# Kernel tuning notes

Measured on AMD Instinct MI355X. Metric: run time of the kernel, lower is better.

Reference implementation:

```python
import jax, jax.numpy as jnp
import numpy as np

TAU = 0.07  # args.density_tau

N, D = 8192, 768   # feature bank
B = 4096           # classify queries
P = 2048           # density peaks
C = 256            # num_class
K_NEIGH = 20       # args.density_k


def setup_inputs() -> dict:
    key = jax.random.key(0)
    k1, k2, k3, k4 = jax.random.split(key, 4)
    return {
        "features": jax.random.normal(k1, (N, D), dtype=jnp.float32),
        "h_i": jax.random.normal(k2, (B, D), dtype=jnp.float32),
        "peak_features": jax.random.normal(k3, (P, D), dtype=jnp.float32),
        "labels": jax.random.randint(k4, (P,), 0, C),
        "K": K_NEIGH,
        "num_class": C,
    }


def _l2norm(x):
    return x / jnp.linalg.norm(x, axis=-1, keepdims=True)


def reference(features, h_i, peak_features, labels, K, num_class):
    # ---- calculate_density_batch ----
    # cosine similarity of every row vs every row: [N, N]
    f = _l2norm(features)
    sim = f @ f.T
    # sort descending + keep K+1 == top_k(K+1); row i's best match is itself
    knn_sims, knn_idx = jax.lax.top_k(sim, K + 1)
    densities = knn_sims[:, 1:].mean(axis=1)   # [N], self excluded
    knn_indices = knn_idx[:, 1:]               # [N, K]
    # density peak test (vectorized find_density_peaks): i is a peak iff
    # its density exceeds all of its K neighbors' densities
    peak_mask = jnp.all(densities[:, None] > densities[knn_indices], axis=1)

    # ---- classify / soft_nearest_neighbor ----
    hn = _l2norm(h_i)
    pn = _l2norm(peak_features)  # cached peak features are L2-normalized
    logits = (hn @ pn.T) / TAU                     # [B, P]
    one_hot = jax.nn.one_hot(labels, num_class, dtype=logits.dtype)  # [P, C]
    # exp(logits) @ one_hot / sum(exp(logits)) == softmax(logits) @ one_hot
    preds = jax.nn.softmax(logits, axis=-1) @ one_hot  # [B, C]

    return preds, densities, knn_indices, peak_mask
```

## Files before the change

### kernel.cpp

```cpp
#include <hip/hip_runtime.h>
#include <math.h>

#define N_FEAT 8192
#define DIM    768
#define B_H    4096
#define P_PK   2048
#define C_CLS  256
#define KNN    20

#define OUT_DENS_OFF  (B_H * C_CLS)
#define OUT_KNN_OFF   (OUT_DENS_OFF + N_FEAT)
#define OUT_MASK_OFF  (OUT_KNN_OFF + N_FEAT * KNN)

typedef __attribute__((ext_vector_type(8)))  short short8b;
typedef __attribute__((ext_vector_type(16))) float f32x16;

__global__ __launch_bounds__(256) void norm64_kernel(const float* __restrict__ X,
    float* __restrict__ nrm, float* __restrict__ rn, int rows) {
  int w    = (int)((blockIdx.x * blockDim.x + threadIdx.x) >> 6);
  int lane = threadIdx.x & 63;
  if (w >= rows) return;
  const float* x = X + (size_t)w * DIM;
  double s = 0.0;
#pragma unroll
  for (int k = 0; k < 12; ++k) {
    float v = x[lane + 64 * k];
    s += (double)v * (double)v;
  }
#pragma unroll
  for (int off = 32; off; off >>= 1) s += __shfl_xor(s, off);
  if (lane == 0) {
    float n32 = (float)sqrt(s);
    nrm[w] = n32;
    rn[w]  = 1.0f / n32;
  }
}

__device__ inline unsigned short f2bf(float x) {
  unsigned u = __float_as_uint(x);
  return (unsigned short)((u + 0x7fffu + ((u >> 16) & 1u)) >> 16);
}

__global__ __launch_bounds__(256) void tobf16_kernel(const float* __restrict__ F,
    const float* __restrict__ rn, unsigned short* __restrict__ fnb) {
  int gid = (blockIdx.x * 256 + threadIdx.x) * 8;
  int row = gid / DIM;
  float s = rn[row];
  float4 v0 = *(const float4*)(F + gid);
  float4 v1 = *(const float4*)(F + gid + 4);
  uint4 o;
  o.x = (unsigned)f2bf(v0.x * s) | ((unsigned)f2bf(v0.y * s) << 16);
  o.y = (unsigned)f2bf(v0.z * s) | ((unsigned)f2bf(v0.w * s) << 16);
  o.z = (unsigned)f2bf(v1.x * s) | ((unsigned)f2bf(v1.y * s) << 16);
  o.w = (unsigned)f2bf(v1.z * s) | ((unsigned)f2bf(v1.w * s) << 16);
  *(uint4*)(fnb + gid) = o;
}

__global__ __launch_bounds__(256) void tofn32_kernel(const float* __restrict__ F,
    const float* __restrict__ nrm, float* __restrict__ fn32) {
#pragma clang fp contract(off)
  int gid = (blockIdx.x * 256 + threadIdx.x) * 4;
  int row = gid / DIM;
  float ni = nrm[row];
  float4 v = *(const float4*)(F + gid);
  v.x = v.x / ni; v.y = v.y / ni; v.z = v.z / ni; v.w = v.w / ni;
  *(float4*)(fn32 + gid) = v;
}

__global__ __launch_bounds__(512, 2) void sim_topk_mfma(
    const unsigned short* __restrict__ fnb, int* __restrict__ cand) {
  __shared__ __align__(16) uint4 Bs[2][128 * 17];
  __shared__ __align__(16) float simb[64][130];

  const int t  = threadIdx.x;
  const int l  = t & 63;
  const int w  = t >> 6;
  const int wr = w >> 2;
  const int wc = w & 3;
  const int rg = blockIdx.x >> 1;
  const int hg = blockIdx.x & 1;
  const int ib = rg * 64;
  const int jb0 = hg * 4096;

  const int lc = l & 31;
  const int lh = l >> 5;
  const int bsw = 4 * (lc & 3);

  const int scol = t >> 2;
  const int sq   = t & 3;
  const int wsw  = sq ^ (scol & 3);

  short8b a[48];
  {
    const unsigned short* ap = fnb + (size_t)(ib + wr * 32 + lc) * DIM + lh * 8;
#pragma unroll
    for (int kc = 0; kc < 48; ++kc) a[kc] = *(const short8b*)(ap + kc * 16);
  }

  const int h = l >> 5;
  const int q = l & 31;
  float lv[4], cmv[4];
  int   li[4];
#pragma unroll
  for (int p = 0; p < 4; ++p) { lv[p] = -3e38f; li[p] = 0; cmv[p] = -3e38f; }

  uint4 v0, v1, v2, v3;
  {
    const unsigned short* gb = fnb + (size_t)(jb0 + scol) * DIM + sq * 32;
    v0 = *(const uint4*)(gb);
    v1 = *(const uint4*)(gb + 8);
    v2 = *(const uint4*)(gb + 16);
    v3 = *(const uint4*)(gb + 24);
  }
  int cur = 0;

#pragma unroll 1
  for (int ct = 0; ct < 32; ++ct) {
    f32x16 acc;
#pragma unroll
    for (int i = 0; i < 16; ++i) acc[i] = 0.f;

#pragma unroll
    for (int kq = 0; kq < 6; ++kq) {
      {
        uint4* bd = &Bs[cur][scol * 17 + 4 * wsw];
        bd[0] = v0; bd[1] = v1; bd[2] = v2; bd[3] = v3;
      }
      __syncthreads();
      if (!(ct == 31 && kq == 5)) {
        const int nct = (kq == 5) ? ct + 1 : ct;
        const int nkq = (kq == 5) ? 0 : kq + 1;
        const unsigned short* gb =
            fnb + (size_t)(jb0 + nct * 128 + scol) * DIM + nkq * 128 + sq * 32;
        v0 = *(const uint4*)(gb);
        v1 = *(const uint4*)(gb + 8);
        v2 = *(const uint4*)(gb + 16);
        v3 = *(const uint4*)(gb + 24);
      }
#pragma unroll
      for (int s = 0; s < 8; ++s) {
        const int slot = (2 * s + lh) ^ bsw;
        const short8b b = *(const short8b*)&Bs[cur][(wc * 32 + lc) * 17 + slot];
        acc = __builtin_amdgcn_mfma_f32_32x32x16_bf16(a[kq * 8 + s], b, acc, 0, 0, 0);
      }
      cur ^= 1;
    }

#pragma unroll
    for (int reg = 0; reg < 16; ++reg) {
      simb[wr * 32 + (reg & 3) + 8 * (reg >> 2) + 4 * lh][wc * 32 + lc] = acc[reg];
    }
    __syncthreads();

    const int jbct = jb0 + ct * 128;
#pragma unroll
    for (int p = 0; p < 4; ++p) {
      const int r  = w * 8 + 2 * p + h;
      const int ig = ib + r;
#pragma unroll
      for (int s = 0; s < 4; ++s) {
        float v  = simb[r][32 * s + q];
        int   jj = jbct + 32 * s + q;
        bool pred = (v > cmv[p]) && (jj != ig);
        unsigned long long bm = __ballot(pred);
        unsigned hm = (unsigned)(bm >> (h * 32));
        while (hm) {
          const int lb = __ffs(hm) - 1;
          hm &= hm - 1;
          const float bv = __shfl(v,  h * 32 + lb);
          const int   bj = __shfl(jj, h * 32 + lb);
          if (bv > cmv[p]) {
            unsigned em = (unsigned)(__ballot(lv[p] == cmv[p]) >> (h * 32));
            if (q == __ffs(em) - 1) { lv[p] = bv; li[p] = bj; }
            float ov = lv[p];
#pragma unroll
            for (int d = 1; d <= 16; d <<= 1) ov = fminf(ov, __shfl_xor(ov, d));
            cmv[p] = ov;
          }
        }
      }
    }
  }

#pragma unroll
  for (int p = 0; p < 4; ++p) {
    const int ig = ib + w * 8 + 2 * p + h;
    cand[(size_t)ig * 64 + hg * 32 + q] = li[p];
  }
}

__global__ __launch_bounds__(256) void refine64_fn32(const float* __restrict__ fn32,
    const int* __restrict__ cand, float* __restrict__ dens, float* __restrict__ knnf) {
#pragma clang fp contract(off)
  const int i = blockIdx.x;
  const int t = threadIdx.x;
  const int l = t & 63;
  const int w = t >> 6;
  __shared__ __align__(16) float fni[DIM];
  __shared__ float s32v[64];
  __shared__ int   vidx[64];
  __shared__ float ssorted[KNN];

  const float* fni_g = fn32 + (size_t)i * DIM;
  for (int d = t; d < DIM; d += 256) fni[d] = fni_g[d];
  if (t < 64) vidx[t] = cand[(size_t)i * 64 + t];
  __syncthreads();

  for (int c = w * 16; c < w * 16 + 16; ++c) {
    const int j = vidx[c];
    const float* fj = fn32 + (size_t)j * DIM;
    double s = 0.0;
#pragma unroll
    for (int k2 = 0; k2 < 12; ++k2) {
      s += (double)fni[l + 64 * k2] * (double)fj[l + 64 * k2];
    }
#pragma unroll
    for (int off = 32; off; off >>= 1) s += __shfl_xor(s, off);
    if (l == 0) s32v[c] = (float)s;
  }
  __syncthreads();

  if (t < 64) {
    const float v = s32v[t];
    const int   j = vidx[t];
    int rank = 0;
    for (int k = 0; k < 64; ++k) {
      float vk = s32v[k]; int jk = vidx[k];
      rank += (vk > v || (vk == v && jk > j)) ? 1 : 0;
    }
    if (rank < KNN) {
      knnf[(size_t)i * KNN + rank] = (float)j;
      ssorted[rank] = v;
    }
  }
  __syncthreads();

  if (t == 0) {
    float rr[8];
#pragma unroll
    for (int u = 0; u < 8; ++u) rr[u] = ssorted[u];
#pragma unroll
    for (int u = 0; u < 8; ++u) rr[u] = rr[u] + ssorted[8 + u];
    float res = ((rr[0] + rr[1]) + (rr[2] + rr[3])) + ((rr[4] + rr[5]) + (rr[6] + rr[7]));
    res = res + ssorted[16];
    res = res + ssorted[17];
    res = res + ssorted[18];
    res = res + ssorted[19];
    dens[i] = res / 20.0f;
  }
}

__global__ __launch_bounds__(256) void refine64_div(const float* __restrict__ F,
    const float* __restrict__ nrm, const int* __restrict__ cand,
    float* __restrict__ dens, float* __restrict__ knnf) {
#pragma clang fp contract(off)
  const int i = blockIdx.x;
  const int t = threadIdx.x;
  const int l = t & 63;
  const int w = t >> 6;
  __shared__ __align__(16) float fni[DIM];
  __shared__ float s32v[64];
  __shared__ int   vidx[64];
  __shared__ float ssorted[KNN];

  const float ni = nrm[i];
  for (int d = t; d < DIM; d += 256) fni[d] = F[(size_t)i * DIM + d] / ni;
  if (t < 64) vidx[t] = cand[(size_t)i * 64 + t];
  __syncthreads();

  for (int c = w * 16; c < w * 16 + 16; ++c) {
    const int j = vidx[c];
    const float* fj = F + (size_t)j * DIM;
    const float nj = nrm[j];
    double s = 0.0;
#pragma unroll
    for (int k2 = 0; k2 < 12; ++k2) {
      float fjn = fj[l + 64 * k2] / nj;
      s += (double)fni[l + 64 * k2] * (double)fjn;
    }
#pragma unroll
    for (int off = 32; off; off >>= 1) s += __shfl_xor(s, off);
    if (l == 0) s32v[c] = (float)s;
  }
  __syncthreads();

  if (t < 64) {
    const float v = s32v[t];
    const int   j = vidx[t];
    int rank = 0;
    for (int k = 0; k < 64; ++k) {
      float vk = s32v[k]; int jk = vidx[k];
      rank += (vk > v || (vk == v && jk > j)) ? 1 : 0;
    }
    if (rank < KNN) {
      knnf[(size_t)i * KNN + rank] = (float)j;
      ssorted[rank] = v;
    }
  }
  __syncthreads();

  if (t == 0) {
    float rr[8];
#pragma unroll
    for (int u = 0; u < 8; ++u) rr[u] = ssorted[u];
#pragma unroll
    for (int u = 0; u < 8; ++u) rr[u] = rr[u] + ssorted[8 + u];
    float res = ((rr[0] + rr[1]) + (rr[2] + rr[3])) + ((rr[4] + rr[5]) + (rr[6] + rr[7]));
    res = res + ssorted[16];
    res = res + ssorted[17];
    res = res + ssorted[18];
    res = res + ssorted[19];
    dens[i] = res / 20.0f;
  }
}

__global__ __launch_bounds__(256) void peak_kernel(const float* __restrict__ dens,
    const float* __restrict__ knnf, float* __restrict__ mask) {
  int i = blockIdx.x * 256 + threadIdx.x;
  if (i >= N_FEAT) return;
  float di = dens[i];
  int ok = 1;
#pragma unroll
  for (int k = 0; k < KNN; ++k) {
    int j = (int)knnf[(size_t)i * KNN + k];
    ok &= (di > dens[j]) ? 1 : 0;
  }
  mask[i] = ok ? 1.0f : 0.0f;
}

__global__ __launch_bounds__(256) void preds_kernel(const float* __restrict__ H,
    const float* __restrict__ Pk, const int* __restrict__ labels,
    const float* __restrict__ rnh, const float* __restrict__ rnp,
    float* __restrict__ outp) {
  __shared__ __align__(16) float Hs[32][12];
  __shared__ __align__(16) float Ps[32][130];
  __shared__ float accc[8][C_CLS];

  const int t  = threadIdx.x;
  const int hb = blockIdx.x * 8;
  const int tx = t & 63;
  const int ry = t >> 6;
  const int hr  = t >> 5;
  const int hkk = t & 31;
  const int pr  = t >> 1;
  const int pkk = (t & 1) * 16;
  const float hrn = rnh[hb + hr];

  for (int i = t; i < 8 * C_CLS; i += 256) ((float*)accc)[i] = 0.f;

  float m[2]    = {-3e38f, -3e38f};
  float ssum[2] = {0.f, 0.f};
  __syncthreads();

  for (int pt = 0; pt < 16; ++pt) {
    const int pb = pt * 128;
    const float prn = rnp[pb + pr];
    float acc[2][2] = {{0.f, 0.f}, {0.f, 0.f}};

    for (int kc = 0; kc < 24; ++kc) {
      const int kb = kc * 32;
      __syncthreads();
      Hs[hkk][hr] = H[(size_t)(hb + hr) * DIM + kb + hkk] * hrn;
      {
        const float* src = Pk + (size_t)(pb + pr) * DIM + kb + pkk;
        float4 v0 = *(const float4*)(src);
        float4 v1 = *(const float4*)(src + 4);
        float4 v2 = *(const float4*)(src + 8);
        float4 v3 = *(const float4*)(src + 12);
        Ps[pkk +  0][pr] = v0.x * prn;  Ps[pkk +  1][pr] = v0.y * prn;
        Ps[pkk +  2][pr] = v0.z * prn;  Ps[pkk +  3][pr] = v0.w * prn;
        Ps[pkk +  4][pr] = v1.x * prn;  Ps[pkk +  5][pr] = v1.y * prn;
        Ps[pkk +  6][pr] = v1.z * prn;  Ps[pkk +  7][pr] = v1.w * prn;
        Ps[pkk +  8][pr] = v2.x * prn;  Ps[pkk +  9][pr] = v2.y * prn;
        Ps[pkk + 10][pr] = v2.z * prn;  Ps[pkk + 11][pr] = v2.w * prn;
        Ps[pkk + 12][pr] = v3.x * prn;  Ps[pkk + 13][pr] = v3.y * prn;
        Ps[pkk + 14][pr] = v3.z * prn;  Ps[pkk + 15][pr] = v3.w * prn;
      }
      __syncthreads();
#pragma unroll
      for (int k = 0; k < 32; ++k) {
        float2 a = *(const float2*)&Hs[k][2 * ry];
        float2 b = *(const float2*)&Ps[k][2 * tx];
        acc[0][0] += a.x * b.x; acc[0][1] += a.x * b.y;
        acc[1][0] += a.y * b.x; acc[1][1] += a.y * b.y;
      }
    }
    const int lab0 = labels[pb + 2 * tx];
    const int lab1 = labels[pb + 2 * tx + 1];
#pragma unroll
    for (int rr = 0; rr < 2; ++rr) {
      float l0 = acc[rr][0] / 0.07f;
      float l1 = acc[rr][1] / 0.07f;
      float tm = fmaxf(l0, l1);
#pragma unroll
      for (int off = 32; off; off >>= 1) tm = fmaxf(tm, __shfl_xor(tm, off));
      float mn = fmaxf(m[rr], tm);
      float sc = expf(m[rr] - mn);
      const int row = 2 * ry + rr;
#pragma unroll
      for (int qq = 0; qq < 4; ++qq) accc[row][tx + 64 * qq] *= sc;
      float e0 = expf(l0 - mn);
      float e1 = expf(l1 - mn);
      float es = e0 + e1;
#pragma unroll
      for (int off = 32; off; off >>= 1) es += __shfl_xor(es, off);
      ssum[rr] = ssum[rr] * sc + es;
      m[rr] = mn;
      atomicAdd(&accc[row][lab0], e0);
      atomicAdd(&accc[row][lab1], e1);
    }
  }
#pragma unroll
  for (int rr = 0; rr < 2; ++rr) {
    const int row = 2 * ry + rr;
    float inv = 1.0f / ssum[rr];
#pragma unroll
    for (int qq = 0; qq < 4; ++qq) {
      outp[(size_t)(hb + row) * C_CLS + tx + 64 * qq] = accc[row][tx + 64 * qq] * inv;
    }
  }
}

extern "C" void kernel_launch(void* const* d_in, const int* in_sizes, int n_in,
                              void* d_out, int out_size, void* d_ws, size_t ws_size,
                              hipStream_t stream) {
  (void)in_sizes; (void)n_in; (void)out_size;
  const float* F      = (const float*)d_in[0];
  const float* H      = (const float*)d_in[1];
  const float* Pk     = (const float*)d_in[2];
  const int*   labels = (const int*)d_in[3];
  float* out = (float*)d_out;

  float* ws   = (float*)d_ws;
  float* nrmF = ws;
  float* rnF  = nrmF + N_FEAT;
  float* nrmH = rnF + N_FEAT;
  float* rnH  = nrmH + B_H;
  float* nrmP = rnH + B_H;
  float* rnP  = nrmP + P_PK;
  int*   cand = (int*)(rnP + P_PK);
  unsigned short* fnb = (unsigned short*)(cand + N_FEAT * 64);
  float* fn32 = (float*)(fnb + (size_t)N_FEAT * DIM);
  const size_t need = (size_t)(fn32 - ws) * 4 + (size_t)N_FEAT * DIM * 4;
  const bool use_fn32 = ws_size >= need;

  norm64_kernel<<<N_FEAT / 4, 256, 0, stream>>>(F, nrmF, rnF, N_FEAT);
  norm64_kernel<<<B_H / 4,  256, 0, stream>>>(H, nrmH, rnH, B_H);
  norm64_kernel<<<P_PK / 4, 256, 0, stream>>>(Pk, nrmP, rnP, P_PK);

  tobf16_kernel<<<N_FEAT * DIM / (8 * 256), 256, 0, stream>>>(F, rnF, fnb);
  if (use_fn32) {
    tofn32_kernel<<<N_FEAT * DIM / (4 * 256), 256, 0, stream>>>(F, nrmF, fn32);
  }

  sim_topk_mfma<<<256, 512, 0, stream>>>(fnb, cand);

  if (use_fn32) {
    refine64_fn32<<<N_FEAT, 256, 0, stream>>>(fn32, cand,
        out + OUT_DENS_OFF, out + OUT_KNN_OFF);
  } else {
    refine64_div<<<N_FEAT, 256, 0, stream>>>(F, nrmF, cand,
        out + OUT_DENS_OFF, out + OUT_KNN_OFF);
  }

  peak_kernel<<<N_FEAT / 256, 256, 0, stream>>>(out + OUT_DENS_OFF,
      out + OUT_KNN_OFF, out + OUT_MASK_OFF);

  preds_kernel<<<B_H / 8, 256, 0, stream>>>(H, Pk, labels, rnH, rnP, out);
}
```

Baseline: 1.374 ms.

## Compute classifier logits with bf16 MFMA using hi/lo split queries

Replaces the scalar FP32 preds kernel with an MFMA-based kernel. Normalized queries are split into bf16 hi and lo parts, and peaks are cast to bf16. Logits are accumulated with two MFMAs per k-chunk, followed by an online softmax and an LDS atomic scatter into class bins. This moves the B×P×D dot products onto matrix cores, at the cost of reduced precision on the peak side and extra workspace and conversion kernels. It falls back to the old kernel when the workspace is too small.

```diff
diff --git a/kernel.cpp b/kernel.cpp
--- a/kernel.cpp
+++ b/kernel.cpp
@@ -13,6 +13,7 @@
 #define OUT_MASK_OFF  (OUT_KNN_OFF + N_FEAT * KNN)
 
 typedef __attribute__((ext_vector_type(8)))  short short8b;
+typedef __attribute__((ext_vector_type(4)))  float f32x4;
 typedef __attribute__((ext_vector_type(16))) float f32x16;
 
 __global__ __launch_bounds__(256) void norm64_kernel(const float* __restrict__ X,
@@ -39,6 +40,9 @@
 __device__ inline unsigned short f2bf(float x) {
   unsigned u = __float_as_uint(x);
   return (unsigned short)((u + 0x7fffu + ((u >> 16) & 1u)) >> 16);
+}
+__device__ inline float bf2f(unsigned short h) {
+  return __uint_as_float(((unsigned)h) << 16);
 }
 
 __global__ __launch_bounds__(256) void tobf16_kernel(const float* __restrict__ F,
@@ -54,6 +58,31 @@
   o.z = (unsigned)f2bf(v1.x * s) | ((unsigned)f2bf(v1.y * s) << 16);
   o.w = (unsigned)f2bf(v1.z * s) | ((unsigned)f2bf(v1.w * s) << 16);
   *(uint4*)(fnb + gid) = o;
+}
+
+__global__ __launch_bounds__(256) void split_kernel(const float* __restrict__ X,
+    const float* __restrict__ rn, unsigned short* __restrict__ hi,
+    unsigned short* __restrict__ lo) {
+  int gid = (blockIdx.x * 256 + threadIdx.x) * 8;
+  int row = gid / DIM;
+  float s = rn[row];
+  float4 v0 = *(const float4*)(X + gid);
+  float4 v1 = *(const float4*)(X + gid + 4);
+  float x[8] = {v0.x * s, v0.y * s, v0.z * s, v0.w * s,
+                v1.x * s, v1.y * s, v1.z * s, v1.w * s};
+  unsigned short h[8], l[8];
+#pragma unroll
+  for (int i = 0; i < 8; ++i) {
+    h[i] = f2bf(x[i]);
+    l[i] = f2bf(x[i] - bf2f(h[i]));
+  }
+  uint4 oh, ol;
+  oh.x = h[0] | ((unsigned)h[1] << 16); oh.y = h[2] | ((unsigned)h[3] << 16);
+  oh.z = h[4] | ((unsigned)h[5] << 16); oh.w = h[6] | ((unsigned)h[7] << 16);
+  ol.x = l[0] | ((unsigned)l[1] << 16); ol.y = l[2] | ((unsigned)l[3] << 16);
+  ol.z = l[4] | ((unsigned)l[5] << 16); ol.w = l[6] | ((unsigned)l[7] << 16);
+  *(uint4*)(hi + gid) = oh;
+  *(uint4*)(lo + gid) = ol;
 }
 
 __global__ __launch_bounds__(256) void tofn32_kernel(const float* __restrict__ F,
@@ -326,6 +355,110 @@
     ok &= (di > dens[j]) ? 1 : 0;
   }
   mask[i] = ok ? 1.0f : 0.0f;
+}
+
+__global__ __launch_bounds__(512) void preds_mfma(
+    const unsigned short* __restrict__ hh, const unsigned short* __restrict__ hl,
+    const unsigned short* __restrict__ ph, const int* __restrict__ labels,
+    float* __restrict__ outp) {
+  __shared__ __align__(16) unsigned short Bsh[2][128 * 40];
+  __shared__ __align__(16) float logit[16][132];
+  __shared__ float accc[16][C_CLS];
+  __shared__ int   labs[P_PK];
+
+  const int t  = threadIdx.x;
+  const int l  = t & 63;
+  const int w  = t >> 6;
+  const int hb = blockIdx.x * 16;
+  const int lr = l & 15;
+  const int lk = l >> 4;
+
+  short8b Ah[24], Al[24];
+  {
+    const unsigned short* hp = hh + (size_t)(hb + lr) * DIM + lk * 8;
+    const unsigned short* lp = hl + (size_t)(hb + lr) * DIM + lk * 8;
+#pragma unroll
+    for (int kc = 0; kc < 24; ++kc) {
+      Ah[kc] = *(const short8b*)(hp + kc * 32);
+      Al[kc] = *(const short8b*)(lp + kc * 32);
+    }
+  }
+
+  for (int i = t; i < P_PK; i += 512) labs[i] = labels[i];
+  for (int i = t; i < 16 * C_CLS; i += 512) ((float*)accc)[i] = 0.f;
+
+  float m0 = -3e38f, m1 = -3e38f, s0 = 0.f, s1 = 0.f;
+
+  const int scol = t >> 2;
+  const int sseg = t & 3;
+
+  uint4 pv = *(const uint4*)(ph + (size_t)scol * DIM + sseg * 8);
+  int cur = 0;
+  __syncthreads();
+
+#pragma unroll 1
+  for (int ct = 0; ct < 16; ++ct) {
+    f32x4 acc = {0.f, 0.f, 0.f, 0.f};
+
+#pragma unroll 1
+    for (int kc = 0; kc < 24; ++kc) {
+      *(uint4*)&Bsh[cur][scol * 40 + sseg * 8] = pv;
+      __syncthreads();
+      if (!(ct == 15 && kc == 23)) {
+        const int nct = (kc == 23) ? ct + 1 : ct;
+        const int nkc = (kc == 23) ? 0 : kc + 1;
+        pv = *(const uint4*)(ph + (size_t)(nct * 128 + scol) * DIM + nkc * 32 + sseg * 8);
+      }
+      const short8b b = *(const short8b*)&Bsh[cur][(16 * w + lr) * 40 + lk * 8];
+      acc = __builtin_amdgcn_mfma_f32_16x16x32_bf16(Ah[kc], b, acc, 0, 0, 0);
+      acc = __builtin_amdgcn_mfma_f32_16x16x32_bf16(Al[kc], b, acc, 0, 0, 0);
+      cur ^= 1;
+    }
+
+#pragma unroll
+    for (int reg = 0; reg < 4; ++reg) {
+      logit[lk * 4 + reg][16 * w + lr] = acc[reg] / 0.07f;
+    }
+    __syncthreads();
+
+    const int pb = ct * 128;
+    const int lab0 = labs[pb + l];
+    const int lab1 = labs[pb + 64 + l];
+#pragma unroll
+    for (int rr = 0; rr < 2; ++rr) {
+      const int r = 2 * w + rr;
+      float v0 = logit[r][l];
+      float v1 = logit[r][64 + l];
+      float tm = fmaxf(v0, v1);
+#pragma unroll
+      for (int off = 32; off; off >>= 1) tm = fmaxf(tm, __shfl_xor(tm, off));
+      float mo = rr ? m1 : m0;
+      float mn = fmaxf(mo, tm);
+      float sc = expf(mo - mn);
+#pragma unroll
+      for (int qq = 0; qq < 4; ++qq) accc[r][l + 64 * qq] *= sc;
+      float e0 = expf(v0 - mn);
+      float e1 = expf(v1 - mn);
+      float es = e0 + e1;
+#pragma unroll
+      for (int off = 32; off; off >>= 1) es += __shfl_xor(es, off);
+      if (rr) { s1 = s1 * sc + es; m1 = mn; }
+      else    { s0 = s0 * sc + es; m0 = mn; }
+      atomicAdd(&accc[r][lab0], e0);
+      atomicAdd(&accc[r][lab1], e1);
+    }
+    __syncthreads();
+  }
+
+#pragma unroll
+  for (int rr = 0; rr < 2; ++rr) {
+    const int r = 2 * w + rr;
+    const float inv = 1.0f / (rr ? s1 : s0);
+#pragma unroll
+    for (int qq = 0; qq < 4; ++qq) {
+      outp[(size_t)(hb + r) * C_CLS + l + 64 * qq] = accc[r][l + 64 * qq] * inv;
+    }
+  }
 }
 
 __global__ __launch_bounds__(256) void preds_kernel(const float* __restrict__ H,
@@ -440,15 +573,26 @@
   float* rnP  = nrmP + P_PK;
   int*   cand = (int*)(rnP + P_PK);
   unsigned short* fnb = (unsigned short*)(cand + N_FEAT * 64);
-  float* fn32 = (float*)(fnb + (size_t)N_FEAT * DIM);
-  const size_t need = (size_t)(fn32 - ws) * 4 + (size_t)N_FEAT * DIM * 4;
-  const bool use_fn32 = ws_size >= need;
+  unsigned short* hhb = fnb + (size_t)N_FEAT * DIM;
+  unsigned short* hlb = hhb + (size_t)B_H * DIM;
+  unsigned short* phb = hlb + (size_t)B_H * DIM;
+  float* fn32 = (float*)(phb + (size_t)P_PK * DIM);
+
+  const size_t base = (size_t)((char*)phb - (char*)ws);
+  const size_t need_preds = base + (size_t)P_PK * DIM * 2;
+  const size_t need_fn32  = need_preds + (size_t)N_FEAT * DIM * 4;
+  const bool use_preds = ws_size >= need_preds;
+  const bool use_fn32  = ws_size >= need_fn32;
 
   norm64_kernel<<<N_FEAT / 4, 256, 0, stream>>>(F, nrmF, rnF, N_FEAT);
   norm64_kernel<<<B_H / 4,  256, 0, stream>>>(H, nrmH, rnH, B_H);
   norm64_kernel<<<P_PK / 4, 256, 0, stream>>>(Pk, nrmP, rnP, P_PK);
 
   tobf16_kernel<<<N_FEAT * DIM / (8 * 256), 256, 0, stream>>>(F, rnF, fnb);
+  if (use_preds) {
+    split_kernel<<<B_H * DIM / (8 * 256), 256, 0, stream>>>(H, rnH, hhb, hlb);
+    tobf16_kernel<<<P_PK * DIM / (8 * 256), 256, 0, stream>>>(Pk, rnP, phb);
+  }
   if (use_fn32) {
     tofn32_kernel<<<N_FEAT * DIM / (4 * 256), 256, 0, stream>>>(F, nrmF, fn32);
   }
@@ -466,5 +610,9 @@
   peak_kernel<<<N_FEAT / 256, 256, 0, stream>>>(out + OUT_DENS_OFF,
       out + OUT_KNN_OFF, out + OUT_MASK_OFF);
 
-  preds_kernel<<<B_H / 8, 256, 0, stream>>>(H, Pk, labels, rnH, rnP, out);
-}
+  if (use_preds) {
+    preds_mfma<<<B_H / 16, 512, 0, stream>>>(hhb, hlb, phb, labels, out);
+  } else {
+    preds_kernel<<<B_H / 8, 256, 0, stream>>>(H, Pk, labels, rnH, rnP, out);
+  }
+}
```

Result: faster. 1.246 ms (-9.3%).
